# Optimization experiments

Measured on AMD Instinct MI355X. Metric: run time of the kernel, lower is better.

Reference implementation:

```python
import jax, jax.numpy as jnp
import numpy as np

B, N, D = 256, 128, 200   # batch, node tokens, descriptor count (d_desc)
DG, DT, DK, H = 256, 256, 256, 4
DH = DK // H
EPS = 1e-5


def _ln(x, g, b):
    mu = jnp.mean(x, -1, keepdims=True)
    v = jnp.var(x, -1, keepdims=True)
    return (x - mu) * jax.lax.rsqrt(v + EPS) * g + b


def _mh_attn(Q, K, V, key_pad_mask):
    # Q:(B,Tq,DK) K,V:(B,Tk,DK) -> ctx:(B,Tq,DK), scores/attn:(B,H,Tq,Tk)
    Bq, Tq, _ = Q.shape
    Tk = K.shape[1]
    Qh = Q.reshape(Bq, Tq, H, DH)
    Kh = K.reshape(Bq, Tk, H, DH)
    Vh = V.reshape(Bq, Tk, H, DH)
    scores = jnp.einsum('bqhd,bkhd->bhqk', Qh, Kh) / (DH ** 0.5)
    if key_pad_mask is not None:
        scores = jnp.where(key_pad_mask[:, None, None, :], -jnp.inf, scores)
    attn = jax.nn.softmax(scores, axis=-1)
    ctx = jnp.einsum('bhqk,bkhd->bqhd', attn, Vh).reshape(Bq, Tq, DK)
    return ctx, scores, attn


def setup_inputs() -> dict:
    key = jax.random.key(0)
    ks = jax.random.split(key, 20)
    def p(i, shape, s=0.05):
        return jax.random.normal(ks[i], shape, jnp.float32) * s
    return dict(
        node_tokens=jax.random.normal(ks[0], (B, N, DG), jnp.float32),
        desc=jax.random.normal(ks[1], (B, D), jnp.float32),
        node_pad_mask=jax.random.randint(ks[2], (B, N), 0, 2).astype(bool),
        id_emb=p(3, (D, DT)),
        val_w1=p(4, (1, DT // 2)), val_b1=jnp.zeros(DT // 2, jnp.float32),
        val_w2=p(5, (DT // 2, DT)), val_b2=jnp.zeros(DT, jnp.float32),
        tok_ln_g=jnp.ones(DT, jnp.float32), tok_ln_b=jnp.zeros(DT, jnp.float32),
        ln_node_g=jnp.ones(DG, jnp.float32), ln_node_b=jnp.zeros(DG, jnp.float32),
        ln_desc_g=jnp.ones(DT, jnp.float32), ln_desc_b=jnp.zeros(DT, jnp.float32),
        Wq_g=p(6, (DG, DK)), bq_g=jnp.zeros(DK, jnp.float32),
        Wk_g=p(7, (DT, DK)), bk_g=jnp.zeros(DK, jnp.float32),
        Wv_g=p(8, (DT, DK)), bv_g=jnp.zeros(DK, jnp.float32),
        Wq_d=p(9, (DT, DK)), bq_d=jnp.zeros(DK, jnp.float32),
        Wk_d=p(10, (DG, DK)), bk_d=jnp.zeros(DK, jnp.float32),
        Wv_d=p(11, (DG, DK)), bv_d=jnp.zeros(DK, jnp.float32),
        proj_node_w=p(12, (DG, DK)), proj_node_b=jnp.zeros(DK, jnp.float32),
        proj_desc_w=p(13, (DT, DK)), proj_desc_b=jnp.zeros(DK, jnp.float32),
        ln_out_g_g=jnp.ones(DK, jnp.float32), ln_out_g_b=jnp.zeros(DK, jnp.float32),
        ln_out_d_g=jnp.ones(DK, jnp.float32), ln_out_d_b=jnp.zeros(DK, jnp.float32),
    )


def reference(node_tokens, desc, node_pad_mask, id_emb, val_w1, val_b1, val_w2, val_b2,
              tok_ln_g, tok_ln_b, ln_node_g, ln_node_b, ln_desc_g, ln_desc_b,
              Wq_g, bq_g, Wk_g, bk_g, Wv_g, bv_g, Wq_d, bq_d, Wk_d, bk_d, Wv_d, bv_d,
              proj_node_w, proj_node_b, proj_desc_w, proj_desc_b,
              ln_out_g_g, ln_out_g_b, ln_out_d_g, ln_out_d_b):
    # Descriptor tokenizer: per-scalar value MLP + id embedding + LN
    h = jax.nn.relu(desc[..., None] @ val_w1 + val_b1)      # (B,D,DT/2)
    val_emb = h @ val_w2 + val_b2                            # (B,D,DT)
    desc_tks = _ln(val_emb + id_emb, tok_ln_g, tok_ln_b)     # (B,D,DT)

    node_in = _ln(node_tokens, ln_node_g, ln_node_b)
    desc_in = _ln(desc_tks, ln_desc_g, ln_desc_b)

    # nodes attend to desc (no key mask)
    ctx_g, scores_g, attn_g = _mh_attn(node_in @ Wq_g + bq_g,
                                       desc_in @ Wk_g + bk_g,
                                       desc_in @ Wv_g + bv_g, None)
    out_g_tokens = _ln(node_tokens @ proj_node_w + proj_node_b + ctx_g,
                       ln_out_g_g, ln_out_g_b)               # (B,N,DK)
    valid = (~node_pad_mask)[..., None].astype(out_g_tokens.dtype)
    denom = jnp.clip(valid.sum(axis=1), 1.0)
    g_vec = (out_g_tokens * valid).sum(axis=1) / denom       # (B,DK)

    # desc attends to nodes (node pad mask on keys)
    ctx_d, scores_d, attn_d = _mh_attn(desc_in @ Wq_d + bq_d,
                                       node_in @ Wk_d + bk_d,
                                       node_in @ Wv_d + bv_d, node_pad_mask)
    out_d_tokens = _ln(desc_tks @ proj_desc_w + proj_desc_b + ctx_d,
                       ln_out_d_g, ln_out_d_b)               # (B,D,DK)
    d_vec = out_d_tokens.mean(axis=1)                        # (B,DK)

    return (g_vec, d_vec, out_g_tokens, out_d_tokens, scores_g, attn_g, scores_d, attn_d)
```

## Files before the change

### kernel.cpp

```cpp
#include <hip/hip_runtime.h>
#include <cmath>
#include <cfloat>

#define BB 256
#define NN 128
#define DD 200
#define CH 256
#define NH 4
#define QKVS 768

#define BF16_SAFE_MAX 3.0e38f

typedef __attribute__((ext_vector_type(8))) __bf16 bf16x8;
typedef __attribute__((ext_vector_type(4))) __bf16 bf16x4;
typedef __attribute__((ext_vector_type(2))) __bf16 bf16x2;
typedef __attribute__((ext_vector_type(4))) float f32x4;

__device__ __forceinline__ float finclamp(float x) {
  return fminf(fmaxf(x, -BF16_SAFE_MAX), BF16_SAFE_MAX);
}

#define GLOAD_LDS16(gp, lp)                                                    \
  __builtin_amdgcn_global_load_lds(                                            \
      (const __attribute__((address_space(1))) void*)(gp),                     \
      (__attribute__((address_space(3))) void*)(lp), 16, 0, 0)

__device__ __forceinline__ void wred2(float& s, float& ss) {
  #pragma unroll
  for (int o = 1; o < 64; o <<= 1) {
    s += __shfl_xor(s, o);
    ss += __shfl_xor(ss, o);
  }
}

struct W9 { const float* p[9]; };
__global__ __launch_bounds__(256)
void mhca_wconv9(W9 w, __bf16* __restrict__ wt) {
  const int z = blockIdx.z;
  const int K = (z == 0) ? 128 : 256;
  if ((int)blockIdx.x * 64 >= K) return;
  __shared__ float t[64][65];
  const float* W = w.p[z];
  __bf16* Wt = wt + (size_t)z * 65536;
  const int k0 = blockIdx.x * 64, n0 = blockIdx.y * 64;
  const int c = threadIdx.x & 63, r0 = threadIdx.x >> 6;
  #pragma unroll
  for (int r = r0; r < 64; r += 4)
    t[r][c] = W[(size_t)(k0 + r) * 256 + n0 + c];
  __syncthreads();
  #pragma unroll
  for (int r = r0; r < 64; r += 4)
    Wt[(size_t)(n0 + r) * K + k0 + c] = (__bf16)t[c][r];
}

__global__ __launch_bounds__(256)
void mhca_gemm_tok(const float* __restrict__ desc, const float* __restrict__ w1,
                   const float* __restrict__ b1, const __bf16* __restrict__ Wt,
                   const float* __restrict__ bias, __bf16* __restrict__ C) {
  constexpr int K = 128;
  __shared__ char lds[2][2][16384];
  const int tid = threadIdx.x;
  const int lane = tid & 63, w = tid >> 6;
  const int n0 = blockIdx.x * 128, m0 = blockIdx.y * 128;
  const int c = lane & 15, g = lane >> 4;
  const int wr = w >> 1, wc = w & 1;

  const bool isA = (w < 2);
  const int half = isA ? w : (w - 2);
  const char* gsrcB = (const char*)Wt + (size_t)(n0 + half * 64) * (K * 2);
  const int lrow = lane >> 3, s8 = lane & 7;
  const int ksw = (s8 ^ lrow) << 4;

  f32x4 acc[4][4];
  #pragma unroll
  for (int mt = 0; mt < 4; ++mt)
    #pragma unroll
    for (int nt = 0; nt < 4; ++nt) acc[mt][nt] = (f32x4){0.f, 0.f, 0.f, 0.f};

  auto stageA = [&](int buf, int kt) {
    char* Ab = &lds[buf][0][half * 8192];
    const int kk = kt * 64 + s8 * 8;
    float4 wa = *(const float4*)&w1[kk];
    float4 wb = *(const float4*)&w1[kk + 4];
    float4 ba = *(const float4*)&b1[kk];
    float4 bb = *(const float4*)&b1[kk + 4];
    #pragma unroll
    for (int i = 0; i < 8; ++i) {
      const float dv = desc[m0 + half * 64 + i * 8 + lrow];
      bf16x8 av;
      av[0] = (__bf16)fmaxf(dv * wa.x + ba.x, 0.f);
      av[1] = (__bf16)fmaxf(dv * wa.y + ba.y, 0.f);
      av[2] = (__bf16)fmaxf(dv * wa.z + ba.z, 0.f);
      av[3] = (__bf16)fmaxf(dv * wa.w + ba.w, 0.f);
      av[4] = (__bf16)fmaxf(dv * wb.x + bb.x, 0.f);
      av[5] = (__bf16)fmaxf(dv * wb.y + bb.y, 0.f);
      av[6] = (__bf16)fmaxf(dv * wb.z + bb.z, 0.f);
      av[7] = (__bf16)fmaxf(dv * wb.w + bb.w, 0.f);
      *(bf16x8*)(Ab + (i * 8 + lrow) * 128 + ksw) = av;
    }
  };
  auto stageB = [&](int buf, int kt) {
    char* ld = &lds[buf][1][half * 8192];
    const char* gs = gsrcB + kt * 128;
    #pragma unroll
    for (int i = 0; i < 8; ++i)
      GLOAD_LDS16(gs + (size_t)(i * 8 + lrow) * (K * 2) + ksw, ld + i * 1024);
  };

  if (isA) stageA(0, 0); else stageB(0, 0);
  __syncthreads();

  int cur = 0;
  #pragma unroll
  for (int kt = 0; kt < 2; ++kt) {
    if (kt + 1 < 2) { if (isA) stageA(cur ^ 1, 1); else stageB(cur ^ 1, 1); }
    const char* A  = lds[cur][0];
    const char* Bt = lds[cur][1];
    #pragma unroll
    for (int kc = 0; kc < 2; ++kc) {
      const int kb = (kc * 64 + g * 16) ^ ((c & 7) << 4);
      bf16x8 a[4], bv[4];
      #pragma unroll
      for (int mt = 0; mt < 4; ++mt)
        a[mt] = *(const bf16x8*)(A + (wr * 64 + mt * 16 + c) * 128 + kb);
      #pragma unroll
      for (int nt = 0; nt < 4; ++nt)
        bv[nt] = *(const bf16x8*)(Bt + (wc * 64 + nt * 16 + c) * 128 + kb);
      #pragma unroll
      for (int mt = 0; mt < 4; ++mt)
        #pragma unroll
        for (int nt = 0; nt < 4; ++nt)
          acc[mt][nt] = __builtin_amdgcn_mfma_f32_16x16x32_bf16(
              a[mt], bv[nt], acc[mt][nt], 0, 0, 0);
    }
    __syncthreads();
    cur ^= 1;
  }

  #pragma unroll
  for (int nt = 0; nt < 4; ++nt) {
    const int n = n0 + wc * 64 + nt * 16 + c;
    const float bn = bias[n];
    #pragma unroll
    for (int mt = 0; mt < 4; ++mt)
      #pragma unroll
      for (int r = 0; r < 4; ++r) {
        const int m = m0 + wr * 64 + mt * 16 + g * 4 + r;
        C[(size_t)m * CH + n] = (__bf16)(acc[mt][nt][r] + bn);
      }
  }
}

struct G4 {
  const __bf16* X[4]; const __bf16* Wt[4];
  const float* bia[4][3]; __bf16* C[4];
};
__global__ __launch_bounds__(256)
void mhca_gemm4(G4 a) {
  constexpr int K = 256;
  const int y = blockIdx.y;
  int side, my, xlim, SC;
  if (y < 400)      { side = 0; my = y;       xlim = 6; SC = QKVS; }
  else if (y < 656) { side = 1; my = y - 400; xlim = 6; SC = QKVS; }
  else if (y < 912) { side = 2; my = y - 656; xlim = 2; SC = CH;  }
  else              { side = 3; my = y - 912; xlim = 2; SC = CH;  }
  if ((int)blockIdx.x >= xlim) return;

  __shared__ char lds[2][2][16384];
  const int tid = threadIdx.x;
  const int lane = tid & 63, w = tid >> 6;
  const int n0 = blockIdx.x * 128, m0 = my * 128;
  const int c = lane & 15, g = lane >> 4;
  const int wr = w >> 1, wc = w & 1;

  const __bf16* X  = a.X[side];
  const __bf16* Wt = a.Wt[side];
  __bf16* C        = a.C[side];
  const float* bp  = a.bia[side][n0 >> 8];

  const bool isA = (w < 2);
  const int half = isA ? w : (w - 2);
  const char* gsrc0 = (const char*)(isA ? X : Wt) +
                      (size_t)((isA ? m0 : n0) + half * 64) * (size_t)(K * 2);
  const size_t rsb = (size_t)K * 2;
  const int lrow = lane >> 3;
  const int ksw  = ((lane & 7) ^ lrow) << 4;

  f32x4 acc[4][4];
  #pragma unroll
  for (int mt = 0; mt < 4; ++mt)
    #pragma unroll
    for (int nt = 0; nt < 4; ++nt) acc[mt][nt] = (f32x4){0.f, 0.f, 0.f, 0.f};

  {
    char* ld = &lds[0][isA ? 0 : 1][half * 8192];
    #pragma unroll
    for (int i = 0; i < 8; ++i)
      GLOAD_LDS16(gsrc0 + (size_t)(i * 8 + lrow) * rsb + ksw, ld + i * 1024);
  }
  __syncthreads();

  int cur = 0;
  #pragma unroll
  for (int kt = 0; kt < 4; ++kt) {
    if (kt + 1 < 4) {
      const char* gs = gsrc0 + (kt + 1) * 128;
      char* ld = &lds[cur ^ 1][isA ? 0 : 1][half * 8192];
      #pragma unroll
      for (int i = 0; i < 8; ++i)
        GLOAD_LDS16(gs + (size_t)(i * 8 + lrow) * rsb + ksw, ld + i * 1024);
    }
    const char* A  = lds[cur][0];
    const char* Bt = lds[cur][1];
    #pragma unroll
    for (int kc = 0; kc < 2; ++kc) {
      const int kb = (kc * 64 + g * 16) ^ ((c & 7) << 4);
      bf16x8 af[4], bv[4];
      #pragma unroll
      for (int mt = 0; mt < 4; ++mt)
        af[mt] = *(const bf16x8*)(A + (wr * 64 + mt * 16 + c) * 128 + kb);
      #pragma unroll
      for (int nt = 0; nt < 4; ++nt)
        bv[nt] = *(const bf16x8*)(Bt + (wc * 64 + nt * 16 + c) * 128 + kb);
      #pragma unroll
      for (int mt = 0; mt < 4; ++mt)
        #pragma unroll
        for (int nt = 0; nt < 4; ++nt)
          acc[mt][nt] = __builtin_amdgcn_mfma_f32_16x16x32_bf16(
              af[mt], bv[nt], acc[mt][nt], 0, 0, 0);
    }
    __syncthreads();
    cur ^= 1;
  }

  #pragma unroll
  for (int nt = 0; nt < 4; ++nt) {
    const int n = n0 + wc * 64 + nt * 16 + c;
    const float bn = bp[n & 255];
    #pragma unroll
    for (int mt = 0; mt < 4; ++mt)
      #pragma unroll
      for (int r = 0; r < 4; ++r) {
        const int m = m0 + wr * 64 + mt * 16 + g * 4 + r;
        C[(size_t)m * SC + n] = (__bf16)(acc[mt][nt][r] + bn);
      }
  }
}

__global__ __launch_bounds__(256)
void mhca_ln2(const float* __restrict__ node_tokens, const float* __restrict__ lng,
              const float* __restrict__ lnb, __bf16* __restrict__ nodein,
              __bf16* __restrict__ ntok,
              const __bf16* __restrict__ vemb, const float* __restrict__ idemb,
              const float* __restrict__ tg, const float* __restrict__ tb,
              const float* __restrict__ dg, const float* __restrict__ db,
              __bf16* __restrict__ dtks, __bf16* __restrict__ din) {
  const int row = blockIdx.x * 4 + (threadIdx.x >> 6);
  const int t4 = (threadIdx.x & 63) * 4;
  if (row < BB * NN) {
    const size_t base = (size_t)row * CH + t4;
    const float4 v = *(const float4*)&node_tokens[base];
    float s = v.x + v.y + v.z + v.w;
    float ss = v.x * v.x + v.y * v.y + v.z * v.z + v.w * v.w;
    wred2(s, ss);
    const float mu = s * (1.f / 256.f);
    const float rstd = rsqrtf(ss * (1.f / 256.f) - mu * mu + 1e-5f);
    const float4 g4 = *(const float4*)&lng[t4];
    const float4 b4 = *(const float4*)&lnb[t4];
    bf16x4 o, rw;
    o[0] = (__bf16)((v.x - mu) * rstd * g4.x + b4.x);
    o[1] = (__bf16)((v.y - mu) * rstd * g4.y + b4.y);
    o[2] = (__bf16)((v.z - mu) * rstd * g4.z + b4.z);
    o[3] = (__bf16)((v.w - mu) * rstd * g4.w + b4.w);
    rw[0] = (__bf16)v.x; rw[1] = (__bf16)v.y; rw[2] = (__bf16)v.z; rw[3] = (__bf16)v.w;
    *(bf16x4*)&nodein[base] = o;
    *(bf16x4*)&ntok[base] = rw;
  } else {
    const int bd = row - BB * NN;
    const int d = bd % DD;
    const size_t base = (size_t)bd * CH + t4;
    const bf16x4 ve = *(const bf16x4*)&vemb[base];
    const float4 ie = *(const float4*)&idemb[(size_t)d * CH + t4];
    float x[4];
    x[0] = (float)ve[0] + ie.x; x[1] = (float)ve[1] + ie.y;
    x[2] = (float)ve[2] + ie.z; x[3] = (float)ve[3] + ie.w;
    float s = x[0] + x[1] + x[2] + x[3];
    float ss = x[0]*x[0] + x[1]*x[1] + x[2]*x[2] + x[3]*x[3];
    wred2(s, ss);
    float mu = s * (1.f / 256.f);
    float rstd = rsqrtf(ss * (1.f / 256.f) - mu * mu + 1e-5f);
    const float4 tg4 = *(const float4*)&tg[t4];
    const float4 tb4 = *(const float4*)&tb[t4];
    float y[4];
    y[0] = (x[0] - mu) * rstd * tg4.x + tb4.x;
    y[1] = (x[1] - mu) * rstd * tg4.y + tb4.y;
    y[2] = (x[2] - mu) * rstd * tg4.z + tb4.z;
    y[3] = (x[3] - mu) * rstd * tg4.w + tb4.w;
    bf16x4 yo;
    yo[0] = (__bf16)y[0]; yo[1] = (__bf16)y[1];
    yo[2] = (__bf16)y[2]; yo[3] = (__bf16)y[3];
    *(bf16x4*)&dtks[base] = yo;
    float s2 = y[0] + y[1] + y[2] + y[3];
    float ss2 = y[0]*y[0] + y[1]*y[1] + y[2]*y[2] + y[3]*y[3];
    wred2(s2, ss2);
    mu = s2 * (1.f / 256.f);
    rstd = rsqrtf(ss2 * (1.f / 256.f) - mu * mu + 1e-5f);
    const float4 dg4 = *(const float4*)&dg[t4];
    const float4 db4 = *(const float4*)&db[t4];
    bf16x4 dov;
    dov[0] = (__bf16)((y[0] - mu) * rstd * dg4.x + db4.x);
    dov[1] = (__bf16)((y[1] - mu) * rstd * dg4.y + db4.y);
    dov[2] = (__bf16)((y[2] - mu) * rstd * dg4.z + db4.z);
    dov[3] = (__bf16)((y[3] - mu) * rstd * dg4.w + db4.w);
    *(bf16x4*)&din[base] = dov;
  }
}

__device__ __forceinline__ int vswz(int d) { return (d & 7) ^ ((d >> 3) & 7); }

template<int TQ, int TK, bool HASM, int NQC>
__device__ __forceinline__
void xattn_body(char* smem, int b, int h, int zq0,
                const __bf16* __restrict__ Qm, const __bf16* __restrict__ Km,
                const __bf16* __restrict__ Vm, const unsigned char* __restrict__ mask,
                float* __restrict__ scores_out, float* __restrict__ attn_out,
                __bf16* __restrict__ ctx_out) {
  constexpr int NT   = (TK + 15) / 16;
  constexpr int KPAD = ((TK + 31) / 32) * 32;
  constexpr int NCH  = KPAD / 32;
  constexpr int PLD  = KPAD + 8;
  constexpr int KVTB = 512;
  constexpr int EXT16 = (TK + 15) & ~15;

  char* VtL = smem;
  typedef __bf16 PldsT[16][PLD];
  PldsT* Plds = (PldsT*)(smem + 64 * KVTB);

  const int w = threadIdx.x >> 6;
  const int lane = threadIdx.x & 63;
  const int c = lane & 15, g = lane >> 4;

  {
    const __bf16* vb0 = Vm + (size_t)b * TK * QKVS + h * 64;
    for (int i = threadIdx.x; i < (TK / 2) * 8; i += 256) {
      const int p = i >> 3, d0 = (i & 7) * 8;
      const bf16x8 v0 = *(const bf16x8*)(vb0 + (size_t)(2 * p) * QKVS + d0);
      const bf16x8 v1 = *(const bf16x8*)(vb0 + (size_t)(2 * p + 1) * QKVS + d0);
      #pragma unroll
      for (int j = 0; j < 8; ++j) {
        const int d = d0 + j;
        const int byte = d * KVTB + ((((p >> 2) ^ vswz(d)) << 4) | ((4 * p) & 15));
        bf16x2 pr; pr[0] = v0[j]; pr[1] = v1[j];
        *(bf16x2*)&VtL[byte] = pr;
      }
    }
    if constexpr (TK < KPAD) {
      constexpr int S0 = TK / 8;
      constexpr int NS = (KPAD - TK) / 8;
      const bf16x8 z = {};
      for (int i = threadIdx.x; i < 64 * NS; i += 256) {
        const int d = i / NS, s = S0 + i % NS;
        *(bf16x8*)&VtL[d * KVTB + ((s ^ vswz(d)) << 4)] = z;
      }
    }
  }
  __syncthreads();

  const __bf16* kbase = Km + (size_t)b * TK * QKVS + h * 64;
  const int er = lane >> 2, ec = (lane & 3) * 4;

  #pragma unroll
  for (int iq = 0; iq < NQC; ++iq) {
    const int qt = (zq0 + iq) * 4 + w;
    if (qt * 16 >= TQ) continue;
    const int q0 = qt * 16;

    const int qr = min(q0 + c, TQ - 1);
    const __bf16* qrow = Qm + ((size_t)b * TQ + qr) * QKVS + h * 64;
    const bf16x8 a0 = *(const bf16x8*)(qrow + g * 8);
    const bf16x8 a1 = *(const bf16x8*)(qrow + 32 + g * 8);

    f32x4 sacc[NT];
    #pragma unroll
    for (int kt = 0; kt < NT; ++kt) {
      const int krow = min(kt * 16 + c, TK - 1);
      const __bf16* kr = kbase + (size_t)krow * QKVS;
      const bf16x8 b0 = *(const bf16x8*)(kr + g * 8);
      const bf16x8 b1 = *(const bf16x8*)(kr + 32 + g * 8);
      f32x4 s = {0.f, 0.f, 0.f, 0.f};
      s = __builtin_amdgcn_mfma_f32_16x16x32_bf16(a0, b0, s, 0, 0, 0);
      s = __builtin_amdgcn_mfma_f32_16x16x32_bf16(a1, b1, s, 0, 0, 0);
      sacc[kt] = s;
    }

    const size_t sbase = (((size_t)b * NH + h) * TQ + q0) * TK;
    const bool erow_ok = (q0 + er < TQ);

    float mr[4] = {-INFINITY, -INFINITY, -INFINITY, -INFINITY};
    #pragma unroll
    for (int kt = 0; kt < NT; ++kt) {
      const int k = kt * 16 + c;
      const bool vk = (k < TK);
      bool mk = false;
      if (HASM) mk = vk && (mask[b * TK + k] != 0);
      #pragma unroll
      for (int r = 0; r < 4; ++r) {
        const float sv = sacc[kt][r] * 0.125f;
        const float se = (vk && !mk) ? sv : -INFINITY;
        Plds[w][g * 4 + r][k] = (__bf16)(mk ? -BF16_SAFE_MAX : sv);
        sacc[kt][r] = se;
        mr[r] = fmaxf(mr[r], se);
      }
    }
    asm volatile("s_waitcnt lgkmcnt(0)" ::: "memory");
    __builtin_amdgcn_sched_barrier(0);

    if (erow_ok) {
      float* srow = scores_out + sbase + (size_t)er * TK;
      #pragma unroll
      for (int k0 = 0; k0 < EXT16; k0 += 16) {
        if (k0 + ec + 3 < TK) {
          const bf16x4 pv4 = *(const bf16x4*)&Plds[w][er][k0 + ec];
          float4 ov;
          ov.x = (float)pv4[0]; ov.y = (float)pv4[1];
          ov.z = (float)pv4[2]; ov.w = (float)pv4[3];
          *(float4*)&srow[k0 + ec] = ov;
        }
      }
    }

    #pragma unroll
    for (int o = 1; o < 16; o <<= 1)
      #pragma unroll
      for (int r = 0; r < 4; ++r) mr[r] = fmaxf(mr[r], __shfl_xor(mr[r], o));

    float sum[4] = {0.f, 0.f, 0.f, 0.f};
    #pragma unroll
    for (int kt = 0; kt < NT; ++kt)
      #pragma unroll
      for (int r = 0; r < 4; ++r) {
        const float e = (mr[r] > -INFINITY) ? __expf(sacc[kt][r] - mr[r]) : 0.f;
        sacc[kt][r] = e;
        sum[r] += e;
      }
    #pragma unroll
    for (int o = 1; o < 16; o <<= 1)
      #pragma unroll
      for (int r = 0; r < 4; ++r) sum[r] += __shfl_xor(sum[r], o);
    float inv[4];
    #pragma unroll
    for (int r = 0; r < 4; ++r) inv[r] = (sum[r] > 0.f) ? 1.f / sum[r] : 0.f;

    #pragma unroll
    for (int kt = 0; kt < NT; ++kt) {
      const int k = kt * 16 + c;
      #pragma unroll
      for (int r = 0; r < 4; ++r)
        Plds[w][g * 4 + r][k] = (__bf16)(sacc[kt][r] * inv[r]);
    }
    if constexpr (KPAD > NT * 16) {
      #pragma unroll
      for (int r = 0; r < 4; ++r) Plds[w][g * 4 + r][NT * 16 + c] = (__bf16)0.f;
    }
    asm volatile("s_waitcnt lgkmcnt(0)" ::: "memory");
    __builtin_amdgcn_sched_barrier(0);

    if (erow_ok) {
      float* arow = attn_out + sbase + (size_t)er * TK;
      #pragma unroll
      for (int k0 = 0; k0 < EXT16; k0 += 16) {
        if (k0 + ec + 3 < TK) {
          const bf16x4 pv4 = *(const bf16x4*)&Plds[w][er][k0 + ec];
          float4 ov;
          ov.x = (float)pv4[0]; ov.y = (float)pv4[1];
          ov.z = (float)pv4[2]; ov.w = (float)pv4[3];
          *(float4*)&arow[k0 + ec] = ov;
        }
      }
    }

    f32x4 ctx[4];
    #pragma unroll
    for (int nt = 0; nt < 4; ++nt) ctx[nt] = (f32x4){0.f, 0.f, 0.f, 0.f};
    #pragma unroll
    for (int kc = 0; kc < NCH; ++kc) {
      const bf16x8 pa = *(const bf16x8*)&Plds[w][c][kc * 32 + g * 8];
      #pragma unroll
      for (int nt = 0; nt < 4; ++nt) {
        const int d = nt * 16 + c;
        const bf16x8 vb =
            *(const bf16x8*)&VtL[d * KVTB + (((kc * 4 + g) ^ vswz(d)) << 4)];
        ctx[nt] = __builtin_amdgcn_mfma_f32_16x16x32_bf16(pa, vb, ctx[nt], 0, 0, 0);
      }
    }

    #pragma unroll
    for (int nt = 0; nt < 4; ++nt)
      #pragma unroll
      for (int r = 0; r < 4; ++r)
        Plds[w][g * 4 + r][nt * 16 + c] = (__bf16)finclamp(ctx[nt][r]);
    asm volatile("s_waitcnt lgkmcnt(0)" ::: "memory");
    __builtin_amdgcn_sched_barrier(0);
    {
      const int cr = lane >> 2, cc = (lane & 3) * 16;
      if (q0 + cr < TQ) {
        __bf16* crow = ctx_out + ((size_t)b * TQ + q0 + cr) * CH + h * 64 + cc;
        *(bf16x8*)&crow[0] = *(const bf16x8*)&Plds[w][cr][cc];
        *(bf16x8*)&crow[8] = *(const bf16x8*)&Plds[w][cr][cc + 8];
      }
    }
  }
}

__global__ __launch_bounds__(256)
void mhca_xattn_both(const __bf16* __restrict__ nodeQKV,
                     const __bf16* __restrict__ dinQKV,
                     const unsigned char* __restrict__ mask,
                     float* __restrict__ o_sg, float* __restrict__ o_ag,
                     __bf16* __restrict__ ctxg,
                     float* __restrict__ o_sd, float* __restrict__ o_ad,
                     __bf16* __restrict__ ctxd) {
  __shared__ char smem[62464];
  const int b = blockIdx.x, h = blockIdx.y, z = blockIdx.z;
  if (z < 2)
    xattn_body<NN, DD, false, 1>(smem, b, h, z, nodeQKV + 0, dinQKV + 0,
                                 dinQKV + 256, nullptr, o_sg, o_ag, ctxg);
  else
    xattn_body<DD, NN, true, 2>(smem, b, h, (z - 2) * 2, dinQKV + 512,
                                nodeQKV + 256, nodeQKV + 512, mask,
                                o_sd, o_ad, ctxd);
}

__global__ __launch_bounds__(256)
void mhca_olnpool(const __bf16* __restrict__ PN, const __bf16* __restrict__ ctxg,
                  const float* __restrict__ gg, const float* __restrict__ gb,
                  float* __restrict__ outg, const unsigned char* __restrict__ mask,
                  float* __restrict__ gv,
                  const __bf16* __restrict__ PD, const __bf16* __restrict__ ctxd,
                  const float* __restrict__ dgam, const float* __restrict__ dbet,
                  float* __restrict__ outd, float* __restrict__ dv) {
  __shared__ float part[4][256];
  __shared__ float cpart[4];
  const bool isg = (int)blockIdx.x < BB;
  const int b = isg ? blockIdx.x : blockIdx.x - BB;
  const int w = threadIdx.x >> 6, lane = threadIdx.x & 63;
  const int t4 = lane * 4;
  const int R = isg ? NN : DD;
  const __bf16* P  = isg ? PN : PD;
  const __bf16* cx = isg ? ctxg : ctxd;
  const float* ga = isg ? gg : dgam;
  const float* be = isg ? gb : dbet;
  float* o = isg ? outg : outd;
  const float4 g4 = *(const float4*)&ga[t4];
  const float4 b4 = *(const float4*)&be[t4];

  float ps0 = 0.f, ps1 = 0.f, ps2 = 0.f, ps3 = 0.f, cnt = 0.f;
  for (int r = w; r < R; r += 4) {
    const size_t base = ((size_t)b * R + r) * CH + t4;
    const bf16x4 pv = *(const bf16x4*)&P[base];
    const bf16x4 cv = *(const bf16x4*)&cx[base];
    float v0 = (float)pv[0] + (float)cv[0];
    float v1 = (float)pv[1] + (float)cv[1];
    float v2 = (float)pv[2] + (float)cv[2];
    float v3 = (float)pv[3] + (float)cv[3];
    float s = v0 + v1 + v2 + v3;
    float ss = v0*v0 + v1*v1 + v2*v2 + v3*v3;
    wred2(s, ss);
    const float mu = s * (1.f / 256.f);
    const float rstd = rsqrtf(ss * (1.f / 256.f) - mu * mu + 1e-5f);
    float4 ov;
    ov.x = finclamp((v0 - mu) * rstd * g4.x + b4.x);
    ov.y = finclamp((v1 - mu) * rstd * g4.y + b4.y);
    ov.z = finclamp((v2 - mu) * rstd * g4.z + b4.z);
    ov.w = finclamp((v3 - mu) * rstd * g4.w + b4.w);
    *(float4*)&o[base] = ov;
    const bool valid = isg ? (mask[b * NN + r] == 0) : true;
    if (valid) {
      ps0 += ov.x; ps1 += ov.y; ps2 += ov.z; ps3 += ov.w;
      cnt += 1.f;
    }
  }
  part[w][t4 + 0] = ps0; part[w][t4 + 1] = ps1;
  part[w][t4 + 2] = ps2; part[w][t4 + 3] = ps3;
  if (lane == 0) cpart[w] = cnt;
  __syncthreads();
  const int col = threadIdx.x;
  const float s = part[0][col] + part[1][col] + part[2][col] + part[3][col];
  if (isg) {
    const float total = cpart[0] + cpart[1] + cpart[2] + cpart[3];
    gv[(size_t)b * CH + col] = s / fmaxf(total, 1.f);
  } else {
    dv[(size_t)b * CH + col] = s * (1.f / 200.f);
  }
}

extern "C" void kernel_launch(void* const* d_in, const int* in_sizes, int n_in,
                              void* d_out, int out_size, void* d_ws, size_t ws_size,
                              hipStream_t stream) {
  const float* node_tokens = (const float*)d_in[0];
  const float* desc_v      = (const float*)d_in[1];
  const unsigned char* pad = (const unsigned char*)d_in[2];
  const float* id_emb      = (const float*)d_in[3];
  const float* val_w1      = (const float*)d_in[4];
  const float* val_b1      = (const float*)d_in[5];
  const float* val_w2      = (const float*)d_in[6];
  const float* val_b2      = (const float*)d_in[7];
  const float* tok_g       = (const float*)d_in[8];
  const float* tok_b       = (const float*)d_in[9];
  const float* ln_node_g   = (const float*)d_in[10];
  const float* ln_node_b   = (const float*)d_in[11];
  const float* ln_desc_g   = (const float*)d_in[12];
  const float* ln_desc_b   = (const float*)d_in[13];
  const float* Wq_g = (const float*)d_in[14]; const float* bq_g = (const float*)d_in[15];
  const float* Wk_g = (const float*)d_in[16]; const float* bk_g = (const float*)d_in[17];
  const float* Wv_g = (const float*)d_in[18]; const float* bv_g = (const float*)d_in[19];
  const float* Wq_d = (const float*)d_in[20]; const float* bq_d = (const float*)d_in[21];
  const float* Wk_d = (const float*)d_in[22]; const float* bk_d = (const float*)d_in[23];
  const float* Wv_d = (const float*)d_in[24]; const float* bv_d = (const float*)d_in[25];
  const float* pnw  = (const float*)d_in[26]; const float* pnb  = (const float*)d_in[27];
  const float* pdw  = (const float*)d_in[28]; const float* pdb  = (const float*)d_in[29];
  const float* logg = (const float*)d_in[30]; const float* logb = (const float*)d_in[31];
  const float* lodg = (const float*)d_in[32]; const float* lodb = (const float*)d_in[33];

  const size_t NEED = 82083840ull * 4ull;
  if (ws_size < NEED) return;
  float* ws = (float*)d_ws;
  __bf16* vemb_bf   = (__bf16*)ws;
  __bf16* nodein_bf = (__bf16*)(ws + 6553600);
  __bf16* ntok_bf   = (__bf16*)(ws + 10747904);
  __bf16* dtks_bf   = (__bf16*)(ws + 14942208);
  __bf16* din_bf    = (__bf16*)(ws + 21495808);
  __bf16* wt        = (__bf16*)(ws + 28049408);
  __bf16* dinQKV    = (__bf16*)(ws + 28344320);
  __bf16* nodeQKV   = (__bf16*)(ws + 48005120);
  __bf16* PN_bf     = (__bf16*)(ws + 60588032);
  __bf16* PD_bf     = (__bf16*)(ws + 64782336);
  __bf16* ctxg_bf   = (__bf16*)(ws + 71335936);
  __bf16* ctxd_bf   = (__bf16*)(ws + 75530240);

  float* out = (float*)d_out;
  float* o_gvec = out;
  float* o_dvec = out + 65536;
  float* o_outg = out + 131072;
  float* o_outd = out + 8519680;
  float* o_sg   = out + 21626880;
  float* o_ag   = out + 47841280;
  float* o_sd   = out + 74055680;
  float* o_ad   = out + 100270080;

  W9 w9;
  w9.p[0] = val_w2;
  w9.p[1] = Wk_g; w9.p[2] = Wv_g; w9.p[3] = Wq_d;
  w9.p[4] = Wq_g; w9.p[5] = Wk_d; w9.p[6] = Wv_d;
  w9.p[7] = pnw;  w9.p[8] = pdw;
  mhca_wconv9<<<dim3(4, 4, 9), 256, 0, stream>>>(w9, wt);

  mhca_gemm_tok<<<dim3(2, 400), 256, 0, stream>>>(desc_v, val_w1, val_b1,
                                                  wt + 0 * 65536, val_b2, vemb_bf);
  mhca_ln2<<<(BB * NN + BB * DD) / 4, 256, 0, stream>>>(
      node_tokens, ln_node_g, ln_node_b, nodein_bf, ntok_bf,
      vemb_bf, id_emb, tok_g, tok_b, ln_desc_g, ln_desc_b, dtks_bf, din_bf);
  G4 g4;
  g4.X[0] = din_bf;    g4.Wt[0] = wt + 1 * 65536; g4.C[0] = dinQKV;
  g4.bia[0][0] = bk_g; g4.bia[0][1] = bv_g;       g4.bia[0][2] = bq_d;
  g4.X[1] = nodein_bf; g4.Wt[1] = wt + 4 * 65536; g4.C[1] = nodeQKV;
  g4.bia[1][0] = bq_g; g4.bia[1][1] = bk_d;       g4.bia[1][2] = bv_d;
  g4.X[2] = ntok_bf;   g4.Wt[2] = wt + 7 * 65536; g4.C[2] = PN_bf;
  g4.bia[2][0] = pnb;  g4.bia[2][1] = pnb;        g4.bia[2][2] = pnb;
  g4.X[3] = dtks_bf;   g4.Wt[3] = wt + 8 * 65536; g4.C[3] = PD_bf;
  g4.bia[3][0] = pdb;  g4.bia[3][1] = pdb;        g4.bia[3][2] = pdb;
  mhca_gemm4<<<dim3(6, 1312), 256, 0, stream>>>(g4);
  mhca_xattn_both<<<dim3(BB, NH, 4), 256, 0, stream>>>(
      nodeQKV, dinQKV, pad, o_sg, o_ag, ctxg_bf, o_sd, o_ad, ctxd_bf);
  mhca_olnpool<<<2 * BB, 256, 0, stream>>>(
      PN_bf, ctxg_bf, logg, logb, o_outg, pad, o_gvec,
      PD_bf, ctxd_bf, lodg, lodb, o_outd, o_dvec);
}
```

Before: 388.0 us.

## Split cross-attention into two kernels with per-direction LDS sizing and more query chunks per block

Replaces the combined cross-attention kernel, which dispatched on blockIdx.z, with two separate kernels. The desc-to-node kernel now processes all query chunks in one block (NQC=4) and uses a smaller V-transpose LDS stride when keys fit in 128, cutting shared memory to about 33 KB so more blocks fit per CU. The node-to-desc kernel now handles both query chunks per block, so K/V staging happens once instead of twice. In exchange the grid has fewer blocks, each doing more serial work, and there is an extra kernel launch.

```diff
diff --git a/kernel.cpp b/kernel.cpp
--- a/kernel.cpp
+++ b/kernel.cpp
@@ -329,7 +329,7 @@
   constexpr int KPAD = ((TK + 31) / 32) * 32;
   constexpr int NCH  = KPAD / 32;
   constexpr int PLD  = KPAD + 8;
-  constexpr int KVTB = 512;
+  constexpr int KVTB = (KPAD <= 128) ? 256 : 512;
   constexpr int EXT16 = (TK + 15) & ~15;
 
   char* VtL = smem;
@@ -513,22 +513,26 @@
 }
 
 __global__ __launch_bounds__(256)
-void mhca_xattn_both(const __bf16* __restrict__ nodeQKV,
-                     const __bf16* __restrict__ dinQKV,
-                     const unsigned char* __restrict__ mask,
-                     float* __restrict__ o_sg, float* __restrict__ o_ag,
-                     __bf16* __restrict__ ctxg,
-                     float* __restrict__ o_sd, float* __restrict__ o_ad,
-                     __bf16* __restrict__ ctxd) {
+void mhca_xattn_g(const __bf16* __restrict__ nodeQKV,
+                  const __bf16* __restrict__ dinQKV,
+                  float* __restrict__ o_sg, float* __restrict__ o_ag,
+                  __bf16* __restrict__ ctxg) {
   __shared__ char smem[62464];
-  const int b = blockIdx.x, h = blockIdx.y, z = blockIdx.z;
-  if (z < 2)
-    xattn_body<NN, DD, false, 1>(smem, b, h, z, nodeQKV + 0, dinQKV + 0,
-                                 dinQKV + 256, nullptr, o_sg, o_ag, ctxg);
-  else
-    xattn_body<DD, NN, true, 2>(smem, b, h, (z - 2) * 2, dinQKV + 512,
-                                nodeQKV + 256, nodeQKV + 512, mask,
-                                o_sd, o_ad, ctxd);
+  xattn_body<NN, DD, false, 2>(smem, blockIdx.x, blockIdx.y, 0,
+                               nodeQKV + 0, dinQKV + 0, dinQKV + 256,
+                               nullptr, o_sg, o_ag, ctxg);
+}
+
+__global__ __launch_bounds__(256)
+void mhca_xattn_d(const __bf16* __restrict__ nodeQKV,
+                  const __bf16* __restrict__ dinQKV,
+                  const unsigned char* __restrict__ mask,
+                  float* __restrict__ o_sd, float* __restrict__ o_ad,
+                  __bf16* __restrict__ ctxd) {
+  __shared__ char smem[33792];
+  xattn_body<DD, NN, true, 4>(smem, blockIdx.x, blockIdx.y, 0,
+                              dinQKV + 512, nodeQKV + 256, nodeQKV + 512,
+                              mask, o_sd, o_ad, ctxd);
 }
 
 __global__ __launch_bounds__(256)
@@ -670,8 +674,10 @@
   g4.X[3] = dtks_bf;   g4.Wt[3] = wt + 8 * 65536; g4.C[3] = PD_bf;
   g4.bia[3][0] = pdb;  g4.bia[3][1] = pdb;        g4.bia[3][2] = pdb;
   mhca_gemm4<<<dim3(6, 1312), 256, 0, stream>>>(g4);
-  mhca_xattn_both<<<dim3(BB, NH, 4), 256, 0, stream>>>(
-      nodeQKV, dinQKV, pad, o_sg, o_ag, ctxg_bf, o_sd, o_ad, ctxd_bf);
+  mhca_xattn_d<<<dim3(BB, NH), 256, 0, stream>>>(
+      nodeQKV, dinQKV, pad, o_sd, o_ad, ctxd_bf);
+  mhca_xattn_g<<<dim3(BB, NH), 256, 0, stream>>>(
+      nodeQKV, dinQKV, o_sg, o_ag, ctxg_bf);
   mhca_olnpool<<<2 * BB, 256, 0, stream>>>(
       PN_bf, ctxg_bf, logg, logb, o_outg, pad, o_gvec,
       PD_bf, ctxd_bf, lodg, lodb, o_outd, o_dvec);
```

Measured after the change: 401.7 us. +3.5%, slower.
